# Optimization experiments

Hardware: AMD Instinct MI355X
Metric: run time of the kernel (lower is better)

The kernel has to match this reference:

```python
import jax, jax.numpy as jnp
import numpy as np

HEADS = 4
DIM_HEAD = 32
DIM = HEADS * DIM_HEAD  # 128
B, H, W, C = 32, 64, 64, 128
LN_EPS = 1e-5


def setup_inputs() -> dict:
    key = jax.random.key(0)
    k0, k1, k2, k3, k4 = jax.random.split(key, 5)
    x = jax.random.normal(k0, (B, H, W, C), dtype=jnp.float32)
    # 1x1 convs are pointwise dense layers over channels
    w_qkv = jax.random.normal(k1, (C, DIM * 3), dtype=jnp.float32) * (1.0 / np.sqrt(C))
    w_out = jax.random.normal(k2, (DIM, C), dtype=jnp.float32) * (1.0 / np.sqrt(DIM))
    b_out = jax.random.normal(k3, (C,), dtype=jnp.float32) * 0.01
    ln_scale = jnp.ones((C,), dtype=jnp.float32)
    return {"x": x, "w_qkv": w_qkv, "w_out": w_out, "b_out": b_out, "ln_scale": ln_scale}


def reference(x, w_qkv, w_out, b_out, ln_scale):
    b, h, w, c = x.shape
    n = h * w
    # qkv projection (1x1 conv, no bias)
    qkv = jnp.einsum('bhwc,cf->bhwf', x, w_qkv)  # [B,H,W,3*DIM]
    q, k, v = jnp.split(qkv, 3, axis=-1)
    # rearrange 'b x y (h d) -> b (x y) h d'
    q = q.reshape(b, n, HEADS, DIM_HEAD)
    k = k.reshape(b, n, HEADS, DIM_HEAD)
    v = v.reshape(b, n, HEADS, DIM_HEAD)
    q = jax.nn.softmax(q, axis=-1) * (1.0 / np.sqrt(DIM_HEAD))
    k = jax.nn.softmax(k, axis=1)  # softmax over spatial positions
    v = v * (1.0 / n)
    # per-head context: [B, heads, d, e]
    context = jnp.einsum('bnhd,bnhe->bhde', k, v)
    # out: 'b h d e, b n h d -> b h e n', then rearrange 'b h e (x y) -> b x y (h e)'
    out = jnp.einsum('bhde,bnhd->bnhe', context, q)  # [B, n, heads, e]
    out = out.reshape(b, h, w, DIM)  # channel order = (h e), matching rearrange
    # output 1x1 conv (with bias)
    out = jnp.einsum('bhwd,dc->bhwc', out, w_out) + b_out
    # LayerNorm over channels, eps=1e-5, no bias
    mu = jnp.mean(out, axis=-1, keepdims=True)
    var = jnp.mean(jnp.square(out - mu), axis=-1, keepdims=True)
    out = (out - mu) * jax.lax.rsqrt(var + LN_EPS) * ln_scale
    return out
```

## Files before the change

### kernel.cpp

```cpp
#include <hip/hip_runtime.h>
#include <hip/hip_bf16.h>

typedef __attribute__((ext_vector_type(4))) float f32x4;
typedef __attribute__((ext_vector_type(8))) short bf16x8;

#define OFF_QS    0ull
#define OFF_EK    33554432ull
#define OFF_VV    67108864ull
#define OFF_PCTX  100663296ull
#define OFF_PSE   109051904ull
#define OFF_CTXG  109314048ull
#define OFF_WQT   109576192ull
#define OFF_WOT   109674496ull

static __device__ __forceinline__ unsigned short f2bf(float f) {
  unsigned int u = __builtin_bit_cast(unsigned int, f);
  return (unsigned short)((u + 0x7fffu + ((u >> 16) & 1u)) >> 16);
}

static __device__ __forceinline__ void unpack8(uint4 u, float* p) {
  p[0] = __builtin_bit_cast(float, u.x << 16);
  p[1] = __builtin_bit_cast(float, u.x & 0xffff0000u);
  p[2] = __builtin_bit_cast(float, u.y << 16);
  p[3] = __builtin_bit_cast(float, u.y & 0xffff0000u);
  p[4] = __builtin_bit_cast(float, u.z << 16);
  p[5] = __builtin_bit_cast(float, u.z & 0xffff0000u);
  p[6] = __builtin_bit_cast(float, u.w << 16);
  p[7] = __builtin_bit_cast(float, u.w & 0xffff0000u);
}

__global__ __launch_bounds__(256) void k_prep(const float* __restrict__ wqkv,
                                              const float* __restrict__ wout,
                                              unsigned short* __restrict__ wqT,
                                              unsigned short* __restrict__ woT) {
  int idx = blockIdx.x * 256 + threadIdx.x;
  if (idx < 49152) {
    int f = idx >> 7, k = idx & 127;
    wqT[idx] = f2bf(wqkv[k * 384 + f]);
  } else {
    int j = idx - 49152;
    int c = j >> 7, k = j & 127;
    woT[j] = f2bf(wout[k * 128 + c]);
  }
}

__global__ __launch_bounds__(512, 2) void k_qkv(const float* __restrict__ x,
                                                const unsigned short* __restrict__ wqT,
                                                unsigned short* __restrict__ qs,
                                                unsigned short* __restrict__ ek,
                                                unsigned short* __restrict__ vv) {
  extern __shared__ char lds[];
  char* lds_w = lds;
  char* lds_a = lds + 98304;

  const int tid = threadIdx.x;
  const long rowbase = (long)blockIdx.x * 128;

  {
    const int4* src = (const int4*)wqT;
    int4* dst = (int4*)lds_w;
#pragma unroll
    for (int i = 0; i < 12; i++) {
      int u = tid + i * 512;
      dst[u ^ ((u >> 4) & 7)] = src[u];
    }
  }
  {
    const f32x4* src = (const f32x4*)(x + rowbase * 128);
#pragma unroll
    for (int i = 0; i < 8; i++) {
      int u = tid + i * 512;
      f32x4 val = src[u];
      ushort4 bq;
      bq.x = f2bf(val.x); bq.y = f2bf(val.y); bq.z = f2bf(val.z); bq.w = f2bf(val.w);
      int ba = (u * 8) ^ (((u >> 5) & 7) << 4);
      *(ushort4*)(lds_a + ba) = bq;
    }
  }
  __syncthreads();

  const int lane = tid & 63;
  const int g = lane >> 4, c = lane & 15;
  const int wave = tid >> 6;
  const int wm = wave >> 2, wf = wave & 3;

  f32x4 acc[4][6];
#pragma unroll
  for (int mt = 0; mt < 4; mt++)
#pragma unroll
    for (int ft = 0; ft < 6; ft++)
      acc[mt][ft] = (f32x4){0.f, 0.f, 0.f, 0.f};

#pragma unroll
  for (int kk = 0; kk < 4; kk++) {
    const int koff = (kk * 32 + g * 8) * 2;
    bf16x8 af[4], bfrag[6];
#pragma unroll
    for (int mt = 0; mt < 4; mt++) {
      int row = wm * 64 + mt * 16 + c;
      af[mt] = *(const bf16x8*)(lds_a + ((row * 256 + koff) ^ ((row & 7) << 4)));
    }
#pragma unroll
    for (int ft = 0; ft < 6; ft++) {
      int frow = wf * 96 + ft * 16 + c;
      bfrag[ft] = *(const bf16x8*)(lds_w + ((frow * 256 + koff) ^ ((frow & 7) << 4)));
    }
#pragma unroll
    for (int mt = 0; mt < 4; mt++)
#pragma unroll
      for (int ft = 0; ft < 6; ft++)
        acc[mt][ft] = __builtin_amdgcn_mfma_f32_16x16x32_bf16(af[mt], bfrag[ft], acc[mt][ft], 0, 0, 0);
  }
  __syncthreads();

  const float RS32 = 0.17677669529663687f;
#pragma unroll
  for (int ch = 0; ch < 3; ch++) {
    int gc = wf * 96 + ch * 32;
    int sec = gc >> 7;
    int sc = gc & 127;
    char* fb = lds + sec * 32768;
#pragma unroll
    for (int mt = 0; mt < 4; mt++) {
      f32x4 a0 = acc[mt][2 * ch];
      f32x4 a1 = acc[mt][2 * ch + 1];
      int row0 = wm * 64 + mt * 16 + g * 4;
      if (sec == 0) {
#pragma unroll
        for (int r = 0; r < 4; r++) {
          float e0 = __expf(a0[r]), e1 = __expf(a1[r]);
          float s = e0 + e1;
          s += __shfl_xor(s, 1); s += __shfl_xor(s, 2);
          s += __shfl_xor(s, 4); s += __shfl_xor(s, 8);
          float inv = RS32 / s;
          int row = row0 + r;
          *(unsigned short*)(fb + ((row * 256 + (sc + c) * 2)      ^ ((row & 7) << 4))) = f2bf(e0 * inv);
          *(unsigned short*)(fb + ((row * 256 + (sc + c + 16) * 2) ^ ((row & 7) << 4))) = f2bf(e1 * inv);
        }
      } else if (sec == 1) {
#pragma unroll
        for (int r = 0; r < 4; r++) {
          int row = row0 + r;
          *(unsigned short*)(fb + ((row * 256 + (sc + c) * 2)      ^ ((row & 7) << 4))) = f2bf(__expf(a0[r]));
          *(unsigned short*)(fb + ((row * 256 + (sc + c + 16) * 2) ^ ((row & 7) << 4))) = f2bf(__expf(a1[r]));
        }
      } else {
#pragma unroll
        for (int r = 0; r < 4; r++) {
          int row = row0 + r;
          *(unsigned short*)(fb + ((row * 256 + (sc + c) * 2)      ^ ((row & 7) << 4))) = f2bf(a0[r]);
          *(unsigned short*)(fb + ((row * 256 + (sc + c + 16) * 2) ^ ((row & 7) << 4))) = f2bf(a1[r]);
        }
      }
    }
  }
  __syncthreads();

  {
    const long off16 = (long)blockIdx.x * 2048;
#pragma unroll
    for (int i = 0; i < 12; i++) {
      int u = tid + i * 512;
      int sec = u >> 11;
      int w = u & 2047, row = w >> 4;
      int4 val = *(const int4*)(lds + sec * 32768 + ((w * 16) ^ ((row & 7) << 4)));
      int4* dst = (sec == 0) ? (int4*)qs : (sec == 1 ? (int4*)ek : (int4*)vv);
      dst[off16 + w] = val;
    }
  }
}

__global__ __launch_bounds__(256) void k_ctx(const unsigned short* __restrict__ ek,
                                             const unsigned short* __restrict__ vv,
                                             float* __restrict__ pctx,
                                             float* __restrict__ pse) {
  extern __shared__ char lds[];
  float* ekc = (float*)lds;
  float* vcc = (float*)(lds + 32768);

  const int tid = threadIdx.x;
  const int chunk = blockIdx.x, b = blockIdx.y;
  const long row0 = (long)b * 4096 + chunk * 256;
  const int wave = tid >> 6, lane = tid & 63;
  const int d0 = (lane >> 3) * 4, e0 = (lane & 7) * 4;
  const int nn = tid >> 2, part = tid & 3;

  f32x4 acc0 = {0.f,0.f,0.f,0.f}, acc1 = {0.f,0.f,0.f,0.f};
  f32x4 acc2 = {0.f,0.f,0.f,0.f}, acc3 = {0.f,0.f,0.f,0.f};
  f32x4 se   = {0.f,0.f,0.f,0.f};

  for (int s = 0; s < 4; s++) {
    long r = row0 + s * 64 + nn;
#pragma unroll
    for (int h = 0; h < 4; h++) {
      uint4 ue = *(const uint4*)(ek + r * 128 + h * 32 + part * 8);
      uint4 uv = *(const uint4*)(vv + r * 128 + h * 32 + part * 8);
      unpack8(ue, &ekc[(h * 64 + nn) * 32 + part * 8]);
      unpack8(uv, &vcc[(h * 64 + nn) * 32 + part * 8]);
    }
    __syncthreads();
    const float* eb = &ekc[(wave * 64) * 32];
    const float* vb = &vcc[(wave * 64) * 32];
#pragma unroll 4
    for (int n = 0; n < 64; n++) {
      f32x4 ev  = *(const f32x4*)(eb + n * 32 + d0);
      f32x4 v4  = *(const f32x4*)(vb + n * 32 + e0);
      acc0 += ev.x * v4;
      acc1 += ev.y * v4;
      acc2 += ev.z * v4;
      acc3 += ev.w * v4;
      se += ev;
    }
    __syncthreads();
  }
  const long pb = ((long)chunk * 128 + b * 4 + wave) * 1024;
  *(f32x4*)&pctx[pb + (d0 + 0) * 32 + e0] = acc0;
  *(f32x4*)&pctx[pb + (d0 + 1) * 32 + e0] = acc1;
  *(f32x4*)&pctx[pb + (d0 + 2) * 32 + e0] = acc2;
  *(f32x4*)&pctx[pb + (d0 + 3) * 32 + e0] = acc3;
  if ((lane & 7) == 0)
    *(f32x4*)&pse[((long)chunk * 128 + b * 4 + wave) * 32 + d0] = se;
}

__global__ __launch_bounds__(256) void k_ctxred(const float* __restrict__ pctx,
                                                const float* __restrict__ pse,
                                                unsigned short* __restrict__ ctxg) {
  int idx = blockIdx.x * 256 + threadIdx.x;
  int de = idx & 1023, d = de >> 5, bh = idx >> 10;
  float s = 0.f, sume = 0.f;
#pragma unroll
  for (int ch = 0; ch < 16; ch++) {
    s    += pctx[(ch * 128 + bh) * 1024 + de];
    sume += pse[(ch * 128 + bh) * 32 + d];
  }
  ctxg[idx] = f2bf(s / (sume * 4096.0f));
}

__global__ __launch_bounds__(512, 2) void k_out(const unsigned short* __restrict__ qs,
                                                const unsigned short* __restrict__ ctxg,
                                                const unsigned short* __restrict__ woT,
                                                const float* __restrict__ bout,
                                                const float* __restrict__ lnsc,
                                                float* __restrict__ out) {
  extern __shared__ char lds[];
  char* lds_wo = lds;
  char* lds_at = lds + 32768;
  unsigned short* lds_cx = (unsigned short*)(lds + 65536);
  float* lds_bias  = (float*)(lds + 73728);
  float* lds_scale = (float*)(lds + 74240);

  const int tid = threadIdx.x;
  const long rowbase = (long)blockIdx.x * 128;
  const int b = blockIdx.x >> 5;

  {
    const int4* src = (const int4*)woT;
    int4* dst = (int4*)lds_wo;
#pragma unroll
    for (int i = 0; i < 4; i++) {
      int u = tid + i * 512;
      dst[u ^ ((u >> 4) & 7)] = src[u];
    }
  }
  {
    const unsigned int* src = (const unsigned int*)(ctxg + (long)b * 4096);
#pragma unroll
    for (int i = 0; i < 4; i++) {
      int u = tid + i * 512;
      unsigned int w = src[u];
      int j = u * 2;
      int e = j & 31, d = (j >> 5) & 31, h = j >> 10;
      lds_cx[(h * 32 + e) * 32 + d]     = (unsigned short)(w & 0xffffu);
      lds_cx[(h * 32 + e + 1) * 32 + d] = (unsigned short)(w >> 16);
    }
  }
  if (tid < 128) { lds_bias[tid] = bout[tid]; lds_scale[tid] = lnsc[tid]; }
  __syncthreads();

  const int lane = tid & 63, g = lane >> 4, c = lane & 15;
  const int wave = tid >> 6;

  f32x4 acc1[4][2];
#pragma unroll
  for (int h = 0; h < 4; h++) { acc1[h][0] = (f32x4){0.f,0.f,0.f,0.f}; acc1[h][1] = (f32x4){0.f,0.f,0.f,0.f}; }
  const unsigned short* qrow = qs + (rowbase + wave * 16 + c) * 128;
#pragma unroll
  for (int h = 0; h < 4; h++) {
    bf16x8 a = *(const bf16x8*)(qrow + h * 32 + g * 8);
#pragma unroll
    for (int et = 0; et < 2; et++) {
      bf16x8 bq = *(const bf16x8*)(lds_cx + (h * 32 + et * 16 + c) * 32 + g * 8);
      acc1[h][et] = __builtin_amdgcn_mfma_f32_16x16x32_bf16(a, bq, acc1[h][et], 0, 0, 0);
    }
  }
  {
    int rowl = wave * 16 + g * 4;
#pragma unroll
    for (int h = 0; h < 4; h++)
#pragma unroll
      for (int et = 0; et < 2; et++) {
        int col = (2 * h + et) * 16 + c;
#pragma unroll
        for (int r = 0; r < 4; r++) {
          int row = rowl + r;
          int ba = (row * 256 + col * 2) ^ ((row & 7) << 4);
          *(unsigned short*)(lds_at + ba) = f2bf(acc1[h][et][r]);
        }
      }
  }
  __syncthreads();

  f32x4 acc2[8];
#pragma unroll
  for (int ct = 0; ct < 8; ct++) acc2[ct] = (f32x4){0.f,0.f,0.f,0.f};
#pragma unroll
  for (int kk = 0; kk < 4; kk++) {
    int koff = (kk * 32 + g * 8) * 2;
    int arow = wave * 16 + c;
    bf16x8 a = *(const bf16x8*)(lds_at + ((arow * 256 + koff) ^ ((arow & 7) << 4)));
#pragma unroll
    for (int ct = 0; ct < 8; ct++) {
      int wrow = ct * 16 + c;
      bf16x8 bw = *(const bf16x8*)(lds_wo + ((wrow * 256 + koff) ^ ((wrow & 7) << 4)));
      acc2[ct] = __builtin_amdgcn_mfma_f32_16x16x32_bf16(a, bw, acc2[ct], 0, 0, 0);
    }
  }

  float biasv[8], scalev[8];
#pragma unroll
  for (int ct = 0; ct < 8; ct++) { biasv[ct] = lds_bias[ct * 16 + c]; scalev[ct] = lds_scale[ct * 16 + c]; }
#pragma unroll
  for (int ct = 0; ct < 8; ct++)
#pragma unroll
    for (int r = 0; r < 4; r++)
      acc2[ct][r] += biasv[ct];

#pragma unroll
  for (int r = 0; r < 4; r++) {
    float s = 0.f, ss = 0.f;
#pragma unroll
    for (int ct = 0; ct < 8; ct++) { float v = acc2[ct][r]; s += v; ss += v * v; }
    s  += __shfl_xor(s, 1);  s  += __shfl_xor(s, 2);  s  += __shfl_xor(s, 4);  s  += __shfl_xor(s, 8);
    ss += __shfl_xor(ss, 1); ss += __shfl_xor(ss, 2); ss += __shfl_xor(ss, 4); ss += __shfl_xor(ss, 8);
    float mu = s * 0.0078125f;
    float var = ss * 0.0078125f - mu * mu;
    float rstd = rsqrtf(var + 1e-5f);
#pragma unroll
    for (int ct = 0; ct < 8; ct++)
      acc2[ct][r] = (acc2[ct][r] - mu) * rstd * scalev[ct];
  }

#pragma unroll
  for (int half = 0; half < 2; half++) {
    __syncthreads();
    if ((wave >> 2) == half) {
      int rl0 = (wave & 3) * 16 + g * 4;
#pragma unroll
      for (int ct = 0; ct < 8; ct++)
#pragma unroll
        for (int r = 0; r < 4; r++) {
          int rl = rl0 + r;
          *(float*)(lds_at + ((rl * 512 + (ct * 16 + c) * 4) ^ ((rl & 7) << 4))) = acc2[ct][r];
        }
    }
    __syncthreads();
    {
      const long base = (rowbase + half * 64) * 32;
#pragma unroll
      for (int i = 0; i < 4; i++) {
        int u = tid + i * 512;
        int row = u >> 5;
        int4 v = *(const int4*)(lds_at + ((u * 16) ^ ((row & 7) << 4)));
        ((int4*)out)[base + u] = v;
      }
    }
  }
}

extern "C" void kernel_launch(void* const* d_in, const int* in_sizes, int n_in,
                              void* d_out, int out_size, void* d_ws, size_t ws_size,
                              hipStream_t stream) {
  (void)in_sizes; (void)n_in; (void)out_size; (void)ws_size;
  const float* x     = (const float*)d_in[0];
  const float* wqkv  = (const float*)d_in[1];
  const float* wout  = (const float*)d_in[2];
  const float* bo    = (const float*)d_in[3];
  const float* lnsc  = (const float*)d_in[4];
  float* out = (float*)d_out;

  char* ws = (char*)d_ws;
  unsigned short* qs   = (unsigned short*)(ws + OFF_QS);
  unsigned short* ek   = (unsigned short*)(ws + OFF_EK);
  unsigned short* vv   = (unsigned short*)(ws + OFF_VV);
  float*          pctx = (float*)(ws + OFF_PCTX);
  float*          pse  = (float*)(ws + OFF_PSE);
  unsigned short* ctxg = (unsigned short*)(ws + OFF_CTXG);
  unsigned short* wqT  = (unsigned short*)(ws + OFF_WQT);
  unsigned short* woT  = (unsigned short*)(ws + OFF_WOT);

  k_prep<<<dim3(256), dim3(256), 0, stream>>>(wqkv, wout, wqT, woT);
  k_qkv<<<dim3(1024), dim3(512), 131072, stream>>>(x, wqT, qs, ek, vv);
  k_ctx<<<dim3(16, 32), dim3(256), 65536, stream>>>(ek, vv, pctx, pse);
  k_ctxred<<<dim3(512), dim3(256), 0, stream>>>(pctx, pse, ctxg);
  k_out<<<dim3(1024), dim3(512), 74752, stream>>>(qs, ctxg, woT, bo, lnsc, out);
}
```

Baseline: 233.2 us.

## Split QKV projection per section and compute context with MFMA on head-major layout

The QKV kernel now launches one block per (row tile, q/k/v section), so it needs only a third of the weight in LDS and can run at higher occupancy. In exchange, every section block re-reads and re-converts the same x tile. Exp(K) and V are written in a head-major layout so the context kernel can read contiguous per-head slices. The context kernel replaces scalar fp32 FMA accumulation with bf16 MFMA on transposed LDS tiles, which cuts the VALU work for K^T V. This adds scattered 2-byte LDS transpose stores and accumulates the exp-sum from bf16-rounded values.

```diff
diff --git a/kernel.cpp b/kernel.cpp
--- a/kernel.cpp
+++ b/kernel.cpp
@@ -3,6 +3,7 @@
 
 typedef __attribute__((ext_vector_type(4))) float f32x4;
 typedef __attribute__((ext_vector_type(8))) short bf16x8;
+typedef __attribute__((ext_vector_type(8))) unsigned short u16x8;
 
 #define OFF_QS    0ull
 #define OFF_EK    33554432ull
@@ -17,16 +18,8 @@
   unsigned int u = __builtin_bit_cast(unsigned int, f);
   return (unsigned short)((u + 0x7fffu + ((u >> 16) & 1u)) >> 16);
 }
-
-static __device__ __forceinline__ void unpack8(uint4 u, float* p) {
-  p[0] = __builtin_bit_cast(float, u.x << 16);
-  p[1] = __builtin_bit_cast(float, u.x & 0xffff0000u);
-  p[2] = __builtin_bit_cast(float, u.y << 16);
-  p[3] = __builtin_bit_cast(float, u.y & 0xffff0000u);
-  p[4] = __builtin_bit_cast(float, u.z << 16);
-  p[5] = __builtin_bit_cast(float, u.z & 0xffff0000u);
-  p[6] = __builtin_bit_cast(float, u.w << 16);
-  p[7] = __builtin_bit_cast(float, u.w & 0xffff0000u);
+static __device__ __forceinline__ float bf2f(unsigned short v) {
+  return __builtin_bit_cast(float, (unsigned int)v << 16);
 }
 
 __global__ __launch_bounds__(256) void k_prep(const float* __restrict__ wqkv,
@@ -44,25 +37,26 @@
   }
 }
 
-__global__ __launch_bounds__(512, 2) void k_qkv(const float* __restrict__ x,
+__global__ __launch_bounds__(512, 4) void k_qkv(const float* __restrict__ x,
                                                 const unsigned short* __restrict__ wqT,
                                                 unsigned short* __restrict__ qs,
-                                                unsigned short* __restrict__ ek,
-                                                unsigned short* __restrict__ vv) {
+                                                unsigned short* __restrict__ ekh,
+                                                unsigned short* __restrict__ vvh) {
   extern __shared__ char lds[];
   char* lds_w = lds;
-  char* lds_a = lds + 98304;
+  char* lds_a = lds + 32768;
 
   const int tid = threadIdx.x;
-  const long rowbase = (long)blockIdx.x * 128;
+  const int tile = blockIdx.x;
+  const int sec = blockIdx.y;
+  const long rowbase = (long)tile * 128;
 
   {
-    const int4* src = (const int4*)wqT;
-    int4* dst = (int4*)lds_w;
-#pragma unroll
-    for (int i = 0; i < 12; i++) {
-      int u = tid + i * 512;
-      dst[u ^ ((u >> 4) & 7)] = src[u];
+    const int4* src = (const int4*)wqT + sec * 2048;
+#pragma unroll
+    for (int i = 0; i < 4; i++) {
+      int u = tid + i * 512;
+      ((int4*)lds_w)[u ^ ((u >> 4) & 7)] = src[u];
     }
   }
   {
@@ -79,147 +73,182 @@
   }
   __syncthreads();
 
-  const int lane = tid & 63;
-  const int g = lane >> 4, c = lane & 15;
+  const int lane = tid & 63, g = lane >> 4, c = lane & 15;
   const int wave = tid >> 6;
   const int wm = wave >> 2, wf = wave & 3;
 
-  f32x4 acc[4][6];
-#pragma unroll
-  for (int mt = 0; mt < 4; mt++)
-#pragma unroll
-    for (int ft = 0; ft < 6; ft++)
-      acc[mt][ft] = (f32x4){0.f, 0.f, 0.f, 0.f};
+  f32x4 acc[4][2];
+#pragma unroll
+  for (int mt = 0; mt < 4; mt++) { acc[mt][0] = (f32x4){0.f,0.f,0.f,0.f}; acc[mt][1] = (f32x4){0.f,0.f,0.f,0.f}; }
 
 #pragma unroll
   for (int kk = 0; kk < 4; kk++) {
     const int koff = (kk * 32 + g * 8) * 2;
-    bf16x8 af[4], bfrag[6];
+    bf16x8 af[4], bfrag[2];
 #pragma unroll
     for (int mt = 0; mt < 4; mt++) {
       int row = wm * 64 + mt * 16 + c;
       af[mt] = *(const bf16x8*)(lds_a + ((row * 256 + koff) ^ ((row & 7) << 4)));
     }
 #pragma unroll
-    for (int ft = 0; ft < 6; ft++) {
-      int frow = wf * 96 + ft * 16 + c;
+    for (int ft = 0; ft < 2; ft++) {
+      int frow = wf * 32 + ft * 16 + c;
       bfrag[ft] = *(const bf16x8*)(lds_w + ((frow * 256 + koff) ^ ((frow & 7) << 4)));
     }
 #pragma unroll
     for (int mt = 0; mt < 4; mt++)
 #pragma unroll
-      for (int ft = 0; ft < 6; ft++)
+      for (int ft = 0; ft < 2; ft++)
         acc[mt][ft] = __builtin_amdgcn_mfma_f32_16x16x32_bf16(af[mt], bfrag[ft], acc[mt][ft], 0, 0, 0);
   }
   __syncthreads();
 
   const float RS32 = 0.17677669529663687f;
-#pragma unroll
-  for (int ch = 0; ch < 3; ch++) {
-    int gc = wf * 96 + ch * 32;
-    int sec = gc >> 7;
-    int sc = gc & 127;
-    char* fb = lds + sec * 32768;
-#pragma unroll
-    for (int mt = 0; mt < 4; mt++) {
-      f32x4 a0 = acc[mt][2 * ch];
-      f32x4 a1 = acc[mt][2 * ch + 1];
-      int row0 = wm * 64 + mt * 16 + g * 4;
-      if (sec == 0) {
-#pragma unroll
-        for (int r = 0; r < 4; r++) {
-          float e0 = __expf(a0[r]), e1 = __expf(a1[r]);
-          float s = e0 + e1;
-          s += __shfl_xor(s, 1); s += __shfl_xor(s, 2);
-          s += __shfl_xor(s, 4); s += __shfl_xor(s, 8);
-          float inv = RS32 / s;
-          int row = row0 + r;
-          *(unsigned short*)(fb + ((row * 256 + (sc + c) * 2)      ^ ((row & 7) << 4))) = f2bf(e0 * inv);
-          *(unsigned short*)(fb + ((row * 256 + (sc + c + 16) * 2) ^ ((row & 7) << 4))) = f2bf(e1 * inv);
-        }
-      } else if (sec == 1) {
-#pragma unroll
-        for (int r = 0; r < 4; r++) {
-          int row = row0 + r;
-          *(unsigned short*)(fb + ((row * 256 + (sc + c) * 2)      ^ ((row & 7) << 4))) = f2bf(__expf(a0[r]));
-          *(unsigned short*)(fb + ((row * 256 + (sc + c + 16) * 2) ^ ((row & 7) << 4))) = f2bf(__expf(a1[r]));
-        }
-      } else {
-#pragma unroll
-        for (int r = 0; r < 4; r++) {
-          int row = row0 + r;
-          *(unsigned short*)(fb + ((row * 256 + (sc + c) * 2)      ^ ((row & 7) << 4))) = f2bf(a0[r]);
-          *(unsigned short*)(fb + ((row * 256 + (sc + c + 16) * 2) ^ ((row & 7) << 4))) = f2bf(a1[r]);
-        }
+  const int sc = wf * 32;
+#pragma unroll
+  for (int mt = 0; mt < 4; mt++) {
+    f32x4 a0 = acc[mt][0], a1 = acc[mt][1];
+    int row0 = wm * 64 + mt * 16 + g * 4;
+    if (sec == 0) {
+#pragma unroll
+      for (int r = 0; r < 4; r++) {
+        float e0 = __expf(a0[r]), e1 = __expf(a1[r]);
+        float s = e0 + e1;
+        s += __shfl_xor(s, 1); s += __shfl_xor(s, 2);
+        s += __shfl_xor(s, 4); s += __shfl_xor(s, 8);
+        float inv = RS32 / s;
+        int row = row0 + r;
+        *(unsigned short*)(lds + ((row * 256 + (sc + c) * 2)      ^ ((row & 7) << 4))) = f2bf(e0 * inv);
+        *(unsigned short*)(lds + ((row * 256 + (sc + c + 16) * 2) ^ ((row & 7) << 4))) = f2bf(e1 * inv);
+      }
+    } else if (sec == 1) {
+#pragma unroll
+      for (int r = 0; r < 4; r++) {
+        int row = row0 + r;
+        *(unsigned short*)(lds + ((row * 256 + (sc + c) * 2)      ^ ((row & 7) << 4))) = f2bf(__expf(a0[r]));
+        *(unsigned short*)(lds + ((row * 256 + (sc + c + 16) * 2) ^ ((row & 7) << 4))) = f2bf(__expf(a1[r]));
+      }
+    } else {
+#pragma unroll
+      for (int r = 0; r < 4; r++) {
+        int row = row0 + r;
+        *(unsigned short*)(lds + ((row * 256 + (sc + c) * 2)      ^ ((row & 7) << 4))) = f2bf(a0[r]);
+        *(unsigned short*)(lds + ((row * 256 + (sc + c + 16) * 2) ^ ((row & 7) << 4))) = f2bf(a1[r]);
       }
     }
   }
   __syncthreads();
 
-  {
-    const long off16 = (long)blockIdx.x * 2048;
-#pragma unroll
-    for (int i = 0; i < 12; i++) {
-      int u = tid + i * 512;
-      int sec = u >> 11;
-      int w = u & 2047, row = w >> 4;
-      int4 val = *(const int4*)(lds + sec * 32768 + ((w * 16) ^ ((row & 7) << 4)));
-      int4* dst = (sec == 0) ? (int4*)qs : (sec == 1 ? (int4*)ek : (int4*)vv);
-      dst[off16 + w] = val;
-    }
-  }
-}
-
-__global__ __launch_bounds__(256) void k_ctx(const unsigned short* __restrict__ ek,
-                                             const unsigned short* __restrict__ vv,
-                                             float* __restrict__ pctx,
-                                             float* __restrict__ pse) {
+  if (sec == 0) {
+    const long off16 = (long)tile * 2048;
+#pragma unroll
+    for (int i = 0; i < 4; i++) {
+      int u = tid + i * 512;
+      int row = u >> 4;
+      int4 v = *(const int4*)(lds + ((u * 16) ^ ((row & 7) << 4)));
+      ((int4*)qs)[off16 + u] = v;
+    }
+  } else {
+    unsigned short* dsth = (sec == 1) ? ekh : vvh;
+#pragma unroll
+    for (int i = 0; i < 4; i++) {
+      int u = tid + i * 512;
+      int row = u >> 4, col16 = u & 15;
+      int h = col16 >> 2, q4 = col16 & 3;
+      int4 v = *(const int4*)(lds + ((u * 16) ^ ((row & 7) << 4)));
+      long di = ((long)h * 131072 + tile * 128 + row) * 4 + q4;
+      ((int4*)dsth)[di] = v;
+    }
+  }
+}
+
+__global__ __launch_bounds__(256, 4) void k_ctx(const unsigned short* __restrict__ ekh,
+                                                const unsigned short* __restrict__ vvh,
+                                                float* __restrict__ pctx,
+                                                float* __restrict__ pse) {
   extern __shared__ char lds[];
-  float* ekc = (float*)lds;
-  float* vcc = (float*)(lds + 32768);
 
   const int tid = threadIdx.x;
-  const int chunk = blockIdx.x, b = blockIdx.y;
-  const long row0 = (long)b * 4096 + chunk * 256;
-  const int wave = tid >> 6, lane = tid & 63;
-  const int d0 = (lane >> 3) * 4, e0 = (lane & 7) * 4;
-  const int nn = tid >> 2, part = tid & 3;
-
-  f32x4 acc0 = {0.f,0.f,0.f,0.f}, acc1 = {0.f,0.f,0.f,0.f};
-  f32x4 acc2 = {0.f,0.f,0.f,0.f}, acc3 = {0.f,0.f,0.f,0.f};
-  f32x4 se   = {0.f,0.f,0.f,0.f};
-
-  for (int s = 0; s < 4; s++) {
-    long r = row0 + s * 64 + nn;
-#pragma unroll
-    for (int h = 0; h < 4; h++) {
-      uint4 ue = *(const uint4*)(ek + r * 128 + h * 32 + part * 8);
-      uint4 uv = *(const uint4*)(vv + r * 128 + h * 32 + part * 8);
-      unpack8(ue, &ekc[(h * 64 + nn) * 32 + part * 8]);
-      unpack8(uv, &vcc[(h * 64 + nn) * 32 + part * 8]);
+  const int h = blockIdx.x & 3, quarter = blockIdx.x >> 2, b = blockIdx.y;
+  const int wave = tid >> 6, lane = tid & 63, g = lane >> 4, c = lane & 15;
+  const long nbase = (long)b * 4096 + quarter * 1024;
+
+  f32x4 acc[2][2];
+#pragma unroll
+  for (int dt = 0; dt < 2; dt++) { acc[dt][0] = (f32x4){0.f,0.f,0.f,0.f}; acc[dt][1] = (f32x4){0.f,0.f,0.f,0.f}; }
+  float se[2] = {0.f, 0.f};
+
+  for (int sci = 0; sci < 4; sci++) {
+    const long n0 = nbase + sci * 256;
+    const uint4* esrc = (const uint4*)(ekh + ((long)h * 131072 + n0 + tid) * 32);
+    const uint4* vsrc = (const uint4*)(vvh + ((long)h * 131072 + n0 + tid) * 32);
+    uint4 ev[4], vq[4];
+#pragma unroll
+    for (int i = 0; i < 4; i++) { ev[i] = esrc[i]; vq[i] = vsrc[i]; }
+
+    if (sci > 0) __syncthreads();
+
+#pragma unroll
+    for (int i = 0; i < 4; i++) {
+      u16x8 es = __builtin_bit_cast(u16x8, ev[i]);
+      u16x8 vs = __builtin_bit_cast(u16x8, vq[i]);
+#pragma unroll
+      for (int j = 0; j < 8; j++) {
+        int d = i * 8 + j;
+        int ba = (d * 512 + tid * 2) ^ ((d & 7) << 4);
+        *(unsigned short*)(lds + ba)         = es[j];
+        *(unsigned short*)(lds + 16384 + ba) = vs[j];
+      }
     }
     __syncthreads();
-    const float* eb = &ekc[(wave * 64) * 32];
-    const float* vb = &vcc[(wave * 64) * 32];
-#pragma unroll 4
-    for (int n = 0; n < 64; n++) {
-      f32x4 ev  = *(const f32x4*)(eb + n * 32 + d0);
-      f32x4 v4  = *(const f32x4*)(vb + n * 32 + e0);
-      acc0 += ev.x * v4;
-      acc1 += ev.y * v4;
-      acc2 += ev.z * v4;
-      acc3 += ev.w * v4;
-      se += ev;
-    }
-    __syncthreads();
-  }
-  const long pb = ((long)chunk * 128 + b * 4 + wave) * 1024;
-  *(f32x4*)&pctx[pb + (d0 + 0) * 32 + e0] = acc0;
-  *(f32x4*)&pctx[pb + (d0 + 1) * 32 + e0] = acc1;
-  *(f32x4*)&pctx[pb + (d0 + 2) * 32 + e0] = acc2;
-  *(f32x4*)&pctx[pb + (d0 + 3) * 32 + e0] = acc3;
-  if ((lane & 7) == 0)
-    *(f32x4*)&pse[((long)chunk * 128 + b * 4 + wave) * 32 + d0] = se;
+
+#pragma unroll
+    for (int ks = 0; ks < 2; ks++) {
+      const int noff = (wave * 64 + ks * 32 + g * 8) * 2;
+      bf16x8 afr[2], bfr[2];
+#pragma unroll
+      for (int dt = 0; dt < 2; dt++) {
+        int row = dt * 16 + c;
+        afr[dt] = *(const bf16x8*)(lds + ((row * 512 + noff) ^ ((row & 7) << 4)));
+      }
+#pragma unroll
+      for (int et = 0; et < 2; et++) {
+        int row = et * 16 + c;
+        bfr[et] = *(const bf16x8*)(lds + 16384 + ((row * 512 + noff) ^ ((row & 7) << 4)));
+      }
+#pragma unroll
+      for (int dt = 0; dt < 2; dt++)
+#pragma unroll
+        for (int j = 0; j < 8; j++)
+          se[dt] += bf2f((unsigned short)afr[dt][j]);
+#pragma unroll
+      for (int dt = 0; dt < 2; dt++)
+#pragma unroll
+        for (int et = 0; et < 2; et++)
+          acc[dt][et] = __builtin_amdgcn_mfma_f32_16x16x32_bf16(afr[dt], bfr[et], acc[dt][et], 0, 0, 0);
+    }
+  }
+
+  const int p = quarter * 4 + wave;
+  const long pb = ((long)p * 128 + b * 4 + h) * 1024;
+#pragma unroll
+  for (int dt = 0; dt < 2; dt++)
+#pragma unroll
+    for (int et = 0; et < 2; et++)
+#pragma unroll
+      for (int r = 0; r < 4; r++)
+        pctx[pb + (dt * 16 + g * 4 + r) * 32 + et * 16 + c] = acc[dt][et][r];
+
+#pragma unroll
+  for (int dt = 0; dt < 2; dt++) {
+    se[dt] += __shfl_xor(se[dt], 16);
+    se[dt] += __shfl_xor(se[dt], 32);
+  }
+  if (lane < 16) {
+#pragma unroll
+    for (int dt = 0; dt < 2; dt++)
+      pse[((long)p * 128 + b * 4 + h) * 32 + dt * 16 + c] = se[dt];
+  }
 }
 
 __global__ __launch_bounds__(256) void k_ctxred(const float* __restrict__ pctx,
@@ -390,8 +419,8 @@
 
   char* ws = (char*)d_ws;
   unsigned short* qs   = (unsigned short*)(ws + OFF_QS);
-  unsigned short* ek   = (unsigned short*)(ws + OFF_EK);
-  unsigned short* vv   = (unsigned short*)(ws + OFF_VV);
+  unsigned short* ekh  = (unsigned short*)(ws + OFF_EK);
+  unsigned short* vvh  = (unsigned short*)(ws + OFF_VV);
   float*          pctx = (float*)(ws + OFF_PCTX);
   float*          pse  = (float*)(ws + OFF_PSE);
   unsigned short* ctxg = (unsigned short*)(ws + OFF_CTXG);
@@ -399,8 +428,8 @@
   unsigned short* woT  = (unsigned short*)(ws + OFF_WOT);
 
   k_prep<<<dim3(256), dim3(256), 0, stream>>>(wqkv, wout, wqT, woT);
-  k_qkv<<<dim3(1024), dim3(512), 131072, stream>>>(x, wqT, qs, ek, vv);
-  k_ctx<<<dim3(16, 32), dim3(256), 65536, stream>>>(ek, vv, pctx, pse);
+  k_qkv<<<dim3(1024, 3), dim3(512), 65536, stream>>>(x, wqT, qs, ekh, vvh);
+  k_ctx<<<dim3(16, 32), dim3(256), 32768, stream>>>(ekh, vvh, pctx, pse);
   k_ctxred<<<dim3(512), dim3(256), 0, stream>>>(pctx, pse, ctxg);
   k_out<<<dim3(1024), dim3(512), 74752, stream>>>(qs, ctxg, woT, bo, lnsc, out);
 }
```

New measurement: 195.2 us. 1.2x faster.
